# Optimization experiments

Hardware: AMD Instinct MI355X
Metric: run time of the kernel (lower is better)

## Reference

```python
import jax, jax.numpy as jnp
import numpy as np

EMBED_DIM = 1024
NUM_HEADS = 16
D_K = EMBED_DIM // NUM_HEADS
B, T = 4, 2048


def setup_inputs() -> dict:
    key = jax.random.key(0)
    k_x, k_wqkv, k_wo = jax.random.split(key, 3)
    x = jax.random.normal(k_x, (B, T, EMBED_DIM), dtype=jnp.float32)
    # kaiming_normal on torch Linear weight [out,in]: std = sqrt(2/fan_in)=sqrt(2/embed_dim)
    std = np.sqrt(2.0 / EMBED_DIM).astype(np.float32)
    # store weights already transposed to [in, out] for y = x @ W + b
    W_qkv = jax.random.normal(k_wqkv, (EMBED_DIM, 3 * EMBED_DIM), dtype=jnp.float32) * std
    b_qkv = jnp.zeros((3 * EMBED_DIM,), dtype=jnp.float32)
    W_o = jax.random.normal(k_wo, (EMBED_DIM, EMBED_DIM), dtype=jnp.float32) * std
    b_o = jnp.zeros((EMBED_DIM,), dtype=jnp.float32)
    return {"x": x, "W_qkv": W_qkv, "b_qkv": b_qkv, "W_o": W_o, "b_o": b_o}


def reference(x, W_qkv, b_qkv, W_o, b_o):
    Bsz, Tlen, D = x.shape
    qkv = x @ W_qkv + b_qkv                      # [B,T,3D]
    q, k, v = jnp.split(qkv, 3, axis=-1)
    # split heads -> [B,H,T,d_k]
    def heads(t):
        return t.reshape(Bsz, Tlen, NUM_HEADS, D_K).transpose(0, 2, 1, 3)
    q, k, v = heads(q), heads(k), heads(v)
    scores = jnp.einsum('bhqd,bhkd->bhqk', q, k) / jnp.sqrt(jnp.float32(D_K))
    causal = jnp.tril(jnp.ones((Tlen, Tlen), dtype=bool))
    scores = jnp.where(causal[None, None], scores, -jnp.inf)
    attn = jax.nn.softmax(scores, axis=-1)
    out = jnp.einsum('bhqk,bhkd->bhqd', attn, v)  # [B,H,T,d_k]
    out = out.transpose(0, 2, 1, 3).reshape(Bsz, Tlen, D)
    return out @ W_o + b_o
```

## Files before the change

kernel.cpp:

```cpp
#include <hip/hip_runtime.h>
#include <hip/hip_bf16.h>
#include <math.h>

typedef unsigned short u16;
typedef __attribute__((ext_vector_type(8))) short bf16x8;
typedef __attribute__((ext_vector_type(4))) float f32x4;

#define BATCH 4
#define TSEQ  2048
#define HEADS 16
#define DK    64
#define EMB   1024
#define MROWS 8192
#define NQKV  3072
#define PHT   ((size_t)MROWS * EMB)

__device__ __forceinline__ u16 f2bf(float f) {
    union { float f; unsigned int i; } v;
    v.f = f;
    unsigned int x = v.i;
    return (u16)((x + 0x7FFFu + ((x >> 16) & 1u)) >> 16);
}

__device__ __forceinline__ unsigned int pk2bf(float a, float b) {
    float2 f2; f2.x = a; f2.y = b;
    union { __hip_bfloat162 h; unsigned int u; } cv;
    cv.h = __float22bfloat162_rn(f2);
    return cv.u;
}

__device__ __forceinline__ void gl2lds16(const u16* g, u16* l) {
    __builtin_amdgcn_global_load_lds(
        (const __attribute__((address_space(1))) unsigned int*)g,
        (__attribute__((address_space(3))) unsigned int*)l, 16, 0, 0);
}

__global__ __launch_bounds__(256) void convert_x(const float* __restrict__ X,
                                                 u16* __restrict__ Xb) {
    int i = (blockIdx.x * 256 + threadIdx.x) * 4;
    float4 v = *(const float4*)&X[i];
    ushort4 o;
    o.x = f2bf(v.x); o.y = f2bf(v.y); o.z = f2bf(v.z); o.w = f2bf(v.w);
    *(ushort4*)&Xb[i] = o;
}

__global__ __launch_bounds__(256) void transpose_w(const float* __restrict__ W,
                                                   u16* __restrict__ Wt,
                                                   int K, int N) {
    __shared__ float tile[32][33];
    const int tx = threadIdx.x & 31, ty = threadIdx.x >> 5;
    const int bx = blockIdx.x, by = blockIdx.y;
#pragma unroll
    for (int s = 0; s < 4; s++)
        tile[ty + 8 * s][tx] = W[(size_t)(by * 32 + ty + 8 * s) * N + bx * 32 + tx];
    __syncthreads();
#pragma unroll
    for (int s = 0; s < 4; s++)
        Wt[(size_t)(bx * 32 + ty + 8 * s) * K + by * 32 + tx] = f2bf(tile[tx][ty + 8 * s]);
}

template <int KDIM>
__device__ __forceinline__ void gemm_core(const u16* __restrict__ A,
                                          const u16* __restrict__ Bt,
                                          u16* As, u16* Bs,
                                          int m0, int n0, int wm, int wn,
                                          int tid, int lo, int quad,
                                          f32x4 (&acc)[4][4]) {
    for (int k0 = 0; k0 < KDIM; k0 += 32) {
        __syncthreads();
#pragma unroll
        for (int c = 0; c < 2; c++) {
            int chunk = c * 256 + tid;
            int row = chunk >> 2, p = chunk & 3;
            int pg = p ^ ((row >> 1) & 3);
            gl2lds16(A + (size_t)(m0 + row) * KDIM + k0 + pg * 8, As + chunk * 8);
            gl2lds16(Bt + (size_t)(n0 + row) * KDIM + k0 + pg * 8, Bs + chunk * 8);
        }
        __syncthreads();
        bf16x8 af[4], bw[4];
#pragma unroll
        for (int i = 0; i < 4; i++) {
            int r = wm + i * 16 + lo;
            int pp = quad ^ ((r >> 1) & 3);
            af[i] = *(const bf16x8*)&As[r * 32 + pp * 8];
        }
#pragma unroll
        for (int j = 0; j < 4; j++) {
            int r = wn + j * 16 + lo;
            int pp = quad ^ ((r >> 1) & 3);
            bw[j] = *(const bf16x8*)&Bs[r * 32 + pp * 8];
        }
#pragma unroll
        for (int i = 0; i < 4; i++)
#pragma unroll
            for (int j = 0; j < 4; j++)
                acc[i][j] = __builtin_amdgcn_mfma_f32_16x16x32_bf16(
                    af[i], bw[j], acc[i][j], 0, 0, 0);
    }
}

__global__ __launch_bounds__(256) void gemm1_mfma(const u16* __restrict__ A,
                                                  const u16* __restrict__ Bt,
                                                  const float* __restrict__ bias,
                                                  u16* __restrict__ qkv) {
    __shared__ u16 As[128 * 32];
    __shared__ u16 Bs[128 * 32];
    const int tid = threadIdx.x;
    const int lane = tid & 63, wv = tid >> 6;
    const int lo = lane & 15, quad = lane >> 4;
    const int m0 = blockIdx.y * 128, n0 = blockIdx.x * 128;
    const int wm = (wv >> 1) * 64, wn = (wv & 1) * 64;
    const float scale2 = 0.18033688011112042f;
    f32x4 acc[4][4] = {};

    gemm_core<1024>(A, Bt, As, Bs, m0, n0, wm, wn, tid, lo, quad, acc);

    const int whichw = (n0 + wn) >> 10;
    if (whichw == 2) {
#pragma unroll
        for (int i = 0; i < 4; i++) {
            int mb = m0 + wm + i * 16 + quad * 4;
            int b = mb >> 11, t = mb & 2047;
#pragma unroll
            for (int j = 0; j < 4; j++) {
                int n = n0 + wn + j * 16 + lo;
                int rem = n & 1023;
                int h = rem >> 6, d = rem & 63;
                float bn = bias[n];
                ushort4 o;
                o.x = f2bf(acc[i][j][0] + bn);
                o.y = f2bf(acc[i][j][1] + bn);
                o.z = f2bf(acc[i][j][2] + bn);
                o.w = f2bf(acc[i][j][3] + bn);
                *(ushort4*)&qkv[2 * PHT +
                                (((size_t)(b * HEADS + h) * DK + d) * TSEQ + t)] = o;
            }
        }
    } else {
        const float sc = (whichw == 0) ? scale2 : 1.0f;
#pragma unroll
        for (int i = 0; i < 4; i++) {
#pragma unroll
            for (int r = 0; r < 4; r++) {
                int m = m0 + wm + i * 16 + quad * 4 + r;
                int b = m >> 11, t = m & 2047;
#pragma unroll
                for (int j = 0; j < 4; j++) {
                    int n = n0 + wn + j * 16 + lo;
                    float v = (acc[i][j][r] + bias[n]) * sc;
                    int rem = n & 1023;
                    int h = rem >> 6, d = rem & 63;
                    qkv[(size_t)whichw * PHT +
                        (((size_t)(b * HEADS + h) * TSEQ + t) * DK + d)] = f2bf(v);
                }
            }
        }
    }
}

__global__ __launch_bounds__(256) void gemm2_mfma(const u16* __restrict__ A,
                                                  const u16* __restrict__ Bt,
                                                  const float* __restrict__ bias,
                                                  float* __restrict__ out) {
    __shared__ u16 As[128 * 32];
    __shared__ u16 Bs[128 * 32];
    const int tid = threadIdx.x;
    const int lane = tid & 63, wv = tid >> 6;
    const int lo = lane & 15, quad = lane >> 4;
    const int m0 = blockIdx.y * 128, n0 = blockIdx.x * 128;
    const int wm = (wv >> 1) * 64, wn = (wv & 1) * 64;
    f32x4 acc[4][4] = {};

    gemm_core<1024>(A, Bt, As, Bs, m0, n0, wm, wn, tid, lo, quad, acc);

#pragma unroll
    for (int i = 0; i < 4; i++) {
#pragma unroll
        for (int r = 0; r < 4; r++) {
            int m = m0 + wm + i * 16 + quad * 4 + r;
#pragma unroll
            for (int j = 0; j < 4; j++) {
                int n = n0 + wn + j * 16 + lo;
                out[(size_t)m * EMB + n] = acc[i][j][r] + bias[n];
            }
        }
    }
}

__global__ __launch_bounds__(256, 2) void attn_mfma(const u16* __restrict__ Qg,
                                                    const u16* __restrict__ Kg,
                                                    const u16* __restrict__ Vg,
                                                    u16* __restrict__ AO) {
    __shared__ u16 pool[3 * 8192];
    u16* Ks = pool;
    u16* Vt = pool + 8192;
    u16* Rr = pool + 16384;

    const int tid = threadIdx.x;
    const int lane = tid & 63, wv = tid >> 6;
    const int lo = lane & 15, quad = lane >> 4;
    const int pair = blockIdx.x, bh = blockIdx.y;
    const size_t base = (size_t)bh * TSEQ * DK;
    const int b = bh >> 4, h = bh & 15;
    const bf16x8 onesf = {0x3F80, 0x3F80, 0x3F80, 0x3F80,
                          0x3F80, 0x3F80, 0x3F80, 0x3F80};

    for (int qi = 0; qi < 2; qi++) {
        const int qt = qi ? (15 - pair) : pair;
        const int q0 = qt * 128;

        __syncthreads();
#pragma unroll
        for (int c = 0; c < 4; c++) {
            int chunk = c * 256 + tid;
            int row = chunk >> 3, p = chunk & 7;
            int pg = p ^ (row & 7);
            gl2lds16(Qg + base + (size_t)(q0 + row) * DK + pg * 8, Rr + chunk * 8);
        }
        __syncthreads();

        bf16x8 bq[2][2];
#pragma unroll
        for (int i = 0; i < 2; i++)
#pragma unroll
            for (int hh = 0; hh < 2; hh++) {
                int row = wv * 32 + i * 16 + lo;
                int ch = (hh * 4 + quad) ^ (row & 7);
                bq[i][hh] = *(const bf16x8*)&Rr[row * 64 + ch * 8];
            }

        f32x4 O[2][5] = {};

        for (int kt = 0; kt <= qt; kt++) {
            __syncthreads();
#pragma unroll
            for (int c = 0; c < 4; c++) {
                int chunk = c * 256 + tid;
                int row = chunk >> 3, p = chunk & 7;
                int pg = p ^ (row & 7);
                gl2lds16(Kg + base + (size_t)(kt * 128 + row) * DK + pg * 8,
                         Ks + chunk * 8);
            }
#pragma unroll
            for (int c = 0; c < 4; c++) {
                int chunk = c * 256 + tid;
                int row = chunk >> 4, p = chunk & 15;
                int pg = p ^ (row & 15);
                gl2lds16(Vg + base + (size_t)row * TSEQ + kt * 128 + pg * 8,
                         Vt + chunk * 8);
            }
            __syncthreads();

            const bool diag = (kt == qt);
            u16* Ps = Rr + wv * 2048;

#pragma unroll
            for (int jh = 0; jh < 2; jh++) {
                f32x4 st[4][2] = {};
#pragma unroll
                for (int hh = 0; hh < 2; hh++) {
#pragma unroll
                    for (int j2 = 0; j2 < 4; j2++) {
                        int row = (jh * 4 + j2) * 16 + lo;
                        int ch = (hh * 4 + quad) ^ (row & 7);
                        bf16x8 ak = *(const bf16x8*)&Ks[row * 64 + ch * 8];
                        st[j2][0] = __builtin_amdgcn_mfma_f32_16x16x32_bf16(
                            ak, bq[0][hh], st[j2][0], 0, 0, 0);
                        st[j2][1] = __builtin_amdgcn_mfma_f32_16x16x32_bf16(
                            ak, bq[1][hh], st[j2][1], 0, 0, 0);
                    }
                }
#pragma unroll
                for (int j2 = 0; j2 < 4; j2++) {
#pragma unroll
                    for (int i = 0; i < 2; i++) {
                        float e[4];
#pragma unroll
                        for (int r = 0; r < 4; r++)
                            e[r] = __builtin_amdgcn_exp2f(st[j2][i][r]);
                        if (diag) {
                            int qr = q0 + wv * 32 + i * 16 + lo;
                            int kb = kt * 128 + (jh * 4 + j2) * 16 + quad * 4;
#pragma unroll
                            for (int r = 0; r < 4; r++)
                                if (kb + r > qr) e[r] = 0.f;
                        }
                        uint2 w;
                        w.x = pk2bf(e[0], e[1]);
                        w.y = pk2bf(e[2], e[3]);
                        int rowl = i * 16 + lo;
                        int chp = (2 * j2 + (quad >> 1)) ^ (lo & 7);
                        *(uint2*)&Ps[rowl * 64 + chp * 8 + (quad & 1) * 4] = w;
                    }
                }
#pragma unroll
                for (int hp = 0; hp < 2; hp++) {
                    bf16x8 ap[2], bv[4];
#pragma unroll
                    for (int i = 0; i < 2; i++) {
                        int rowl = i * 16 + lo;
                        int ch = (4 * hp + quad) ^ (lo & 7);
                        ap[i] = *(const bf16x8*)&Ps[rowl * 64 + ch * 8];
                    }
#pragma unroll
                    for (int jn = 0; jn < 4; jn++) {
                        int vrow = jn * 16 + lo;
                        int ch = (8 * jh + 4 * hp + quad) ^ (vrow & 15);
                        bv[jn] = *(const bf16x8*)&Vt[vrow * 128 + ch * 8];
                    }
#pragma unroll
                    for (int i = 0; i < 2; i++) {
#pragma unroll
                        for (int jn = 0; jn < 4; jn++)
                            O[i][jn] = __builtin_amdgcn_mfma_f32_16x16x32_bf16(
                                ap[i], bv[jn], O[i][jn], 0, 0, 0);
                        O[i][4] = __builtin_amdgcn_mfma_f32_16x16x32_bf16(
                            ap[i], onesf, O[i][4], 0, 0, 0);
                    }
                }
            }
        }

#pragma unroll
        for (int i = 0; i < 2; i++)
#pragma unroll
            for (int r = 0; r < 4; r++) {
                int qrow = q0 + wv * 32 + i * 16 + quad * 4 + r;
                float inv = 1.f / O[i][4][r];
#pragma unroll
                for (int jn = 0; jn < 4; jn++) {
                    int d = jn * 16 + lo;
                    AO[(((size_t)b * TSEQ + qrow) * HEADS + h) * DK + d] =
                        f2bf(O[i][jn][r] * inv);
                }
            }
    }
}

extern "C" void kernel_launch(void* const* d_in, const int* in_sizes, int n_in,
                              void* d_out, int out_size, void* d_ws, size_t ws_size,
                              hipStream_t stream) {
    const float* x    = (const float*)d_in[0];
    const float* Wqkv = (const float*)d_in[1];
    const float* bqkv = (const float*)d_in[2];
    const float* Wo   = (const float*)d_in[3];
    const float* bo   = (const float*)d_in[4];
    float* out = (float*)d_out;

    u16* Xb  = (u16*)d_ws;
    u16* Wt  = Xb + PHT;
    u16* Wot = Wt + (size_t)NQKV * EMB;
    u16* qkv = Wot + (size_t)EMB * EMB;
    u16* AO  = Xb;

    convert_x<<<MROWS * EMB / 1024, 256, 0, stream>>>(x, Xb);
    transpose_w<<<dim3(NQKV / 32, EMB / 32), 256, 0, stream>>>(Wqkv, Wt, EMB, NQKV);
    transpose_w<<<dim3(EMB / 32, EMB / 32), 256, 0, stream>>>(Wo, Wot, EMB, EMB);

    gemm1_mfma<<<dim3(NQKV / 128, MROWS / 128), 256, 0, stream>>>(Xb, Wt, bqkv, qkv);
    attn_mfma<<<dim3(8, BATCH * HEADS), 256, 0, stream>>>(
        qkv, qkv + PHT, qkv + 2 * PHT, AO);
    gemm2_mfma<<<dim3(EMB / 128, MROWS / 128), 256, 0, stream>>>(AO, Wot, bo, out);
}
```

Baseline: 257.0 us.

## Double-buffer attention K/V tiles, widen GEMM K-step, merge weight transposes

The attention kernel now keeps two K/V buffers in LDS and prefetches the next tile while the current one is computed, which removes one barrier per iteration and hides load latency. The cost is more LDS per block (80KB instead of 48KB), which may cut occupancy. The GEMM core now loads 64-wide K slices per barrier pair instead of 32, halving the synchronisation count, with the swizzle adjusted to match. The two weight-transpose launches are merged into one kernel to save a launch.

```diff
diff --git a/kernel.cpp b/kernel.cpp
--- a/kernel.cpp
+++ b/kernel.cpp
@@ -44,19 +44,26 @@
     *(ushort4*)&Xb[i] = o;
 }
 
-__global__ __launch_bounds__(256) void transpose_w(const float* __restrict__ W,
-                                                   u16* __restrict__ Wt,
-                                                   int K, int N) {
+__global__ __launch_bounds__(256) void transpose_both(const float* __restrict__ Wqkv,
+                                                      const float* __restrict__ Wo,
+                                                      u16* __restrict__ Wt,
+                                                      u16* __restrict__ Wot) {
     __shared__ float tile[32][33];
     const int tx = threadIdx.x & 31, ty = threadIdx.x >> 5;
-    const int bx = blockIdx.x, by = blockIdx.y;
+    const int K = 1024;
+    const float* W;
+    u16* D;
+    int N, bx;
+    if (blockIdx.x < 96) { W = Wqkv; D = Wt; N = 3072; bx = blockIdx.x; }
+    else                 { W = Wo;   D = Wot; N = 1024; bx = blockIdx.x - 96; }
+    const int by = blockIdx.y;
 #pragma unroll
     for (int s = 0; s < 4; s++)
         tile[ty + 8 * s][tx] = W[(size_t)(by * 32 + ty + 8 * s) * N + bx * 32 + tx];
     __syncthreads();
 #pragma unroll
     for (int s = 0; s < 4; s++)
-        Wt[(size_t)(bx * 32 + ty + 8 * s) * K + by * 32 + tx] = f2bf(tile[tx][ty + 8 * s]);
+        D[(size_t)(bx * 32 + ty + 8 * s) * K + by * 32 + tx] = f2bf(tile[tx][ty + 8 * s]);
 }
 
 template <int KDIM>
@@ -66,36 +73,39 @@
                                           int m0, int n0, int wm, int wn,
                                           int tid, int lo, int quad,
                                           f32x4 (&acc)[4][4]) {
-    for (int k0 = 0; k0 < KDIM; k0 += 32) {
+    for (int k0 = 0; k0 < KDIM; k0 += 64) {
         __syncthreads();
 #pragma unroll
-        for (int c = 0; c < 2; c++) {
+        for (int c = 0; c < 4; c++) {
             int chunk = c * 256 + tid;
-            int row = chunk >> 2, p = chunk & 3;
-            int pg = p ^ ((row >> 1) & 3);
+            int row = chunk >> 3, p = chunk & 7;
+            int pg = p ^ (row & 7);
             gl2lds16(A + (size_t)(m0 + row) * KDIM + k0 + pg * 8, As + chunk * 8);
             gl2lds16(Bt + (size_t)(n0 + row) * KDIM + k0 + pg * 8, Bs + chunk * 8);
         }
         __syncthreads();
-        bf16x8 af[4], bw[4];
-#pragma unroll
-        for (int i = 0; i < 4; i++) {
-            int r = wm + i * 16 + lo;
-            int pp = quad ^ ((r >> 1) & 3);
-            af[i] = *(const bf16x8*)&As[r * 32 + pp * 8];
-        }
-#pragma unroll
-        for (int j = 0; j < 4; j++) {
-            int r = wn + j * 16 + lo;
-            int pp = quad ^ ((r >> 1) & 3);
-            bw[j] = *(const bf16x8*)&Bs[r * 32 + pp * 8];
-        }
-#pragma unroll
-        for (int i = 0; i < 4; i++)
-#pragma unroll
-            for (int j = 0; j < 4; j++)
-                acc[i][j] = __builtin_amdgcn_mfma_f32_16x16x32_bf16(
-                    af[i], bw[j], acc[i][j], 0, 0, 0);
+#pragma unroll
+        for (int kk = 0; kk < 2; kk++) {
+            bf16x8 af[4], bw[4];
+#pragma unroll
+            for (int i = 0; i < 4; i++) {
+                int r = wm + i * 16 + lo;
+                int ch = (kk * 4 + quad) ^ (r & 7);
+                af[i] = *(const bf16x8*)&As[r * 64 + ch * 8];
+            }
+#pragma unroll
+            for (int j = 0; j < 4; j++) {
+                int r = wn + j * 16 + lo;
+                int ch = (kk * 4 + quad) ^ (r & 7);
+                bw[j] = *(const bf16x8*)&Bs[r * 64 + ch * 8];
+            }
+#pragma unroll
+            for (int i = 0; i < 4; i++)
+#pragma unroll
+                for (int j = 0; j < 4; j++)
+                    acc[i][j] = __builtin_amdgcn_mfma_f32_16x16x32_bf16(
+                        af[i], bw[j], acc[i][j], 0, 0, 0);
+        }
     }
 }
 
@@ -103,8 +113,8 @@
                                                   const u16* __restrict__ Bt,
                                                   const float* __restrict__ bias,
                                                   u16* __restrict__ qkv) {
-    __shared__ u16 As[128 * 32];
-    __shared__ u16 Bs[128 * 32];
+    __shared__ u16 As[128 * 64];
+    __shared__ u16 Bs[128 * 64];
     const int tid = threadIdx.x;
     const int lane = tid & 63, wv = tid >> 6;
     const int lo = lane & 15, quad = lane >> 4;
@@ -162,8 +172,8 @@
                                                   const u16* __restrict__ Bt,
                                                   const float* __restrict__ bias,
                                                   float* __restrict__ out) {
-    __shared__ u16 As[128 * 32];
-    __shared__ u16 Bs[128 * 32];
+    __shared__ u16 As[128 * 64];
+    __shared__ u16 Bs[128 * 64];
     const int tid = threadIdx.x;
     const int lane = tid & 63, wv = tid >> 6;
     const int lo = lane & 15, quad = lane >> 4;
@@ -191,10 +201,8 @@
                                                     const u16* __restrict__ Kg,
                                                     const u16* __restrict__ Vg,
                                                     u16* __restrict__ AO) {
-    __shared__ u16 pool[3 * 8192];
-    u16* Ks = pool;
-    u16* Vt = pool + 8192;
-    u16* Rr = pool + 16384;
+    __shared__ u16 pool[5 * 8192];
+    u16* Rr = pool + 4 * 8192;
 
     const int tid = threadIdx.x;
     const int lane = tid & 63, wv = tid >> 6;
@@ -205,6 +213,27 @@
     const bf16x8 onesf = {0x3F80, 0x3F80, 0x3F80, 0x3F80,
                           0x3F80, 0x3F80, 0x3F80, 0x3F80};
 
+    auto stageKV = [&](int kt2, int bufsel) {
+        u16* Kd = pool + bufsel * 8192;
+        u16* Vd = pool + 2 * 8192 + bufsel * 8192;
+#pragma unroll
+        for (int c = 0; c < 4; c++) {
+            int chunk = c * 256 + tid;
+            int row = chunk >> 3, p = chunk & 7;
+            int pg = p ^ (row & 7);
+            gl2lds16(Kg + base + (size_t)(kt2 * 128 + row) * DK + pg * 8,
+                     Kd + chunk * 8);
+        }
+#pragma unroll
+        for (int c = 0; c < 4; c++) {
+            int chunk = c * 256 + tid;
+            int row = chunk >> 4, p = chunk & 15;
+            int pg = p ^ (row & 15);
+            gl2lds16(Vg + base + (size_t)row * TSEQ + kt2 * 128 + pg * 8,
+                     Vd + chunk * 8);
+        }
+    };
+
     for (int qi = 0; qi < 2; qi++) {
         const int qt = qi ? (15 - pair) : pair;
         const int q0 = qt * 128;
@@ -217,6 +246,7 @@
             int pg = p ^ (row & 7);
             gl2lds16(Qg + base + (size_t)(q0 + row) * DK + pg * 8, Rr + chunk * 8);
         }
+        stageKV(0, 0);
         __syncthreads();
 
         bf16x8 bq[2][2];
@@ -232,24 +262,11 @@
         f32x4 O[2][5] = {};
 
         for (int kt = 0; kt <= qt; kt++) {
-            __syncthreads();
-#pragma unroll
-            for (int c = 0; c < 4; c++) {
-                int chunk = c * 256 + tid;
-                int row = chunk >> 3, p = chunk & 7;
-                int pg = p ^ (row & 7);
-                gl2lds16(Kg + base + (size_t)(kt * 128 + row) * DK + pg * 8,
-                         Ks + chunk * 8);
-            }
-#pragma unroll
-            for (int c = 0; c < 4; c++) {
-                int chunk = c * 256 + tid;
-                int row = chunk >> 4, p = chunk & 15;
-                int pg = p ^ (row & 15);
-                gl2lds16(Vg + base + (size_t)row * TSEQ + kt * 128 + pg * 8,
-                         Vt + chunk * 8);
-            }
-            __syncthreads();
+            const int cur = kt & 1;
+            if (kt) __syncthreads();
+            if (kt < qt) stageKV(kt + 1, cur ^ 1);
+            const u16* Ksc = pool + cur * 8192;
+            const u16* Vtc = pool + 2 * 8192 + cur * 8192;
 
             const bool diag = (kt == qt);
             u16* Ps = Rr + wv * 2048;
@@ -263,7 +280,7 @@
                     for (int j2 = 0; j2 < 4; j2++) {
                         int row = (jh * 4 + j2) * 16 + lo;
                         int ch = (hh * 4 + quad) ^ (row & 7);
-                        bf16x8 ak = *(const bf16x8*)&Ks[row * 64 + ch * 8];
+                        bf16x8 ak = *(const bf16x8*)&Ksc[row * 64 + ch * 8];
                         st[j2][0] = __builtin_amdgcn_mfma_f32_16x16x32_bf16(
                             ak, bq[0][hh], st[j2][0], 0, 0, 0);
                         st[j2][1] = __builtin_amdgcn_mfma_f32_16x16x32_bf16(
@@ -306,7 +323,7 @@
                     for (int jn = 0; jn < 4; jn++) {
                         int vrow = jn * 16 + lo;
                         int ch = (8 * jh + 4 * hp + quad) ^ (vrow & 15);
-                        bv[jn] = *(const bf16x8*)&Vt[vrow * 128 + ch * 8];
+                        bv[jn] = *(const bf16x8*)&Vtc[vrow * 128 + ch * 8];
                     }
 #pragma unroll
                     for (int i = 0; i < 2; i++) {
@@ -354,8 +371,7 @@
     u16* AO  = Xb;
 
     convert_x<<<MROWS * EMB / 1024, 256, 0, stream>>>(x, Xb);
-    transpose_w<<<dim3(NQKV / 32, EMB / 32), 256, 0, stream>>>(Wqkv, Wt, EMB, NQKV);
-    transpose_w<<<dim3(EMB / 32, EMB / 32), 256, 0, stream>>>(Wo, Wot, EMB, EMB);
+    transpose_both<<<dim3(96 + 32, 32), 256, 0, stream>>>(Wqkv, Wo, Wt, Wot);
 
     gemm1_mfma<<<dim3(NQKV / 128, MROWS / 128), 256, 0, stream>>>(Xb, Wt, bqkv, qkv);
     attn_mfma<<<dim3(8, BATCH * HEADS), 256, 0, stream>>>(
```

New measurement: 295.1 us. 1.15x slower.
